# Kernel tuning notes

Hardware: AMD Instinct MI355X
Metric: run time of the kernel (lower is better)

Reference implementation:

```python
import jax, jax.numpy as jnp
import numpy as np

N_KNOTS = 16384
BATCH = 256
N_SAMP = 32768


def setup_inputs() -> dict:
    key = jax.random.key(0)
    k1, k2, k3 = jax.random.split(key, 3)
    # strictly increasing knot abscissae (matches module assumption of sorted x_points)
    incs = jax.random.uniform(k1, (N_KNOTS,), minval=0.01, maxval=1.0, dtype=jnp.float32)
    x_points = jnp.cumsum(incs)
    y_points = jax.random.normal(k2, (N_KNOTS,), dtype=jnp.float32)
    # samples must have a valid right bracket: x in [x_points[0], x_points[N-2])
    lo = x_points[0]
    hi = x_points[N_KNOTS - 2]
    u = jax.random.uniform(k3, (BATCH, N_SAMP), dtype=jnp.float32)
    x_samp = lo + u * (hi - lo) * 0.999
    return {"x_samp": x_samp, "x_points": x_points, "y_points": y_points}


def reference(x_samp, x_points, y_points):
    # Original: masked argmin over (x_samp - x_points) with negatives set to inf,
    # i.e. index of the largest knot <= x_samp. Equivalent to searchsorted(right)-1.
    idxi = jnp.searchsorted(x_points, x_samp, side='right') - 1  # [B, S]
    idxf = idxi + 1
    xi = x_points[idxi]  # [B, S] gather
    xf = x_points[idxf]
    yi = y_points[idxi]
    yf = y_points[idxf]
    ds = (x_samp - xi) / (xf - xi)
    return yi + ds * (yf - yi)
```

## Files before the change

kernel.cpp:

```cpp
#include <hip/hip_runtime.h>


#define NB 16256
#define NKMAX 16384
#define PADR 4
#define NREC (NKMAX + PADR)

typedef float f32x4 __attribute__((ext_vector_type(4)));
typedef float f32x2 __attribute__((ext_vector_type(2)));

__device__ __forceinline__ int bucket_of(float v, float lo, float inv_w) {
    return (int)((v - lo) * inv_w);
}

__device__ __forceinline__ float pack_ys_f(float y, float s) {
    _Float16 hy = (_Float16)y, hs = (_Float16)s;
    unsigned short uy = __builtin_bit_cast(unsigned short, hy);
    unsigned short us = __builtin_bit_cast(unsigned short, hs);
    unsigned u = (unsigned)uy | ((unsigned)us << 16);
    return __builtin_bit_cast(float, u);
}

__device__ __forceinline__ float lerp_ys(float dx, float ysf) {
    unsigned u = __builtin_bit_cast(unsigned, ysf);
    float hy = (float)__builtin_bit_cast(_Float16, (unsigned short)(u & 0xffffu));
    float hs = (float)__builtin_bit_cast(_Float16, (unsigned short)(u >> 16));
    return fmaf(dx, hs, hy);
}

__global__ void build_tbl(const float* __restrict__ xp, const float* __restrict__ yp,
                          float* __restrict__ recg, unsigned short* __restrict__ tbl,
                          int nk) {
    int i = blockIdx.x * blockDim.x + threadIdx.x;
    float lo = xp[0];
    float inv_w = (float)NB / (xp[nk - 1] - lo);
    if (i < nk + PADR) {
        float x, y, s;
        if (i < nk) {
            x = xp[i]; y = yp[i];
            s = (i < nk - 1) ? (yp[i + 1] - y) / (xp[i + 1] - x) : 0.0f;
        } else {
            x = __builtin_inff(); y = 0.0f; s = 0.0f;
        }
        recg[2 * i]     = x;
        recg[2 * i + 1] = pack_ys_f(y, s);
    }
    if (i < NB) {
        int v = 0;
        if (i > 0) {
            int loj = -1, hij = nk - 1;
            while (loj < hij) {
                int mid = (loj + hij + 1) >> 1;
                if (bucket_of(xp[mid], lo, inv_w) <= i - 1) loj = mid; else hij = mid - 1;
            }
            v = loj < 0 ? 0 : (loj > nk - 2 ? nk - 2 : loj);
        }
        tbl[i] = (unsigned short)v;
    }
}

__global__ __launch_bounds__(1024) void interp(
        const f32x4* __restrict__ xs4, const float* __restrict__ xp,
        const float* __restrict__ recg, const unsigned short* __restrict__ tbl,
        f32x4* __restrict__ out4, int n4, int nk) {
    __shared__ __align__(16) float srec[NREC * 2];
    __shared__ unsigned short sT[NB];

    {
        const f32x4* rg4 = (const f32x4*)recg;
        f32x4* sr4 = (f32x4*)srec;
        int n = (NREC * 2) / 4;
        for (int i = threadIdx.x; i < n; i += 1024) sr4[i] = rg4[i];
        for (int i = threadIdx.x; i < NB; i += 1024) sT[i] = tbl[i];
    }

    float lo = xp[0];
    float inv_w = (float)NB / (xp[nk - 1] - lo);
    __syncthreads();

    const f32x2* sr2 = (const f32x2*)srec;

    int tid = blockIdx.x * blockDim.x + threadIdx.x;
    int T = gridDim.x * blockDim.x;

    auto process = [&](f32x4 xq) -> f32x4 {
        float x[4] = {xq.x, xq.y, xq.z, xq.w};
        int base[4];
        f32x2 r0[4], r1[4], r2[4], r3[4];
        #pragma unroll
        for (int k = 0; k < 4; k++) {
            int b = bucket_of(x[k], lo, inv_w);
            b = min(b, NB - 1);
            base[k] = (int)sT[b];
            r0[k] = sr2[base[k]];
            r1[k] = sr2[base[k] + 1];
            r2[k] = sr2[base[k] + 2];
            r3[k] = sr2[base[k] + 3];
        }
        f32x4 res;
        #pragma unroll
        for (int k = 0; k < 4; k++) {
            float xk = x[k];
            float xi = r0[k].x, ys = r0[k].y;
            if (r1[k].x <= xk) { xi = r1[k].x; ys = r1[k].y; }
            if (r2[k].x <= xk) { xi = r2[k].x; ys = r2[k].y; }
            bool tail = (r3[k].x <= xk);
            if (tail) {
                int j = base[k] + 3;
                while (srec[2 * (j + 1)] <= xk) j++;
                xi = srec[2 * j]; ys = srec[2 * j + 1];
            }
            res[k] = lerp_ys(xk - xi, ys);
        }
        return res;
    };

    if (n4 == 8 * T) {
        f32x4 buf[8];
        #pragma unroll
        for (int s = 0; s < 3; s++)
            buf[s] = __builtin_nontemporal_load(&xs4[tid + s * T]);
        #pragma unroll
        for (int s = 0; s < 8; s++) {
            if (s + 3 < 8)
                buf[s + 3] = __builtin_nontemporal_load(&xs4[tid + (s + 3) * T]);
            f32x4 res = process(buf[s]);
            __builtin_nontemporal_store(res, &out4[tid + s * T]);
        }
    } else {
        for (int t = tid; t < n4; t += T) {
            f32x4 xq = __builtin_nontemporal_load(&xs4[t]);
            f32x4 res = process(xq);
            __builtin_nontemporal_store(res, &out4[t]);
        }
    }
}

extern "C" void kernel_launch(void* const* d_in, const int* in_sizes, int n_in,
                              void* d_out, int out_size, void* d_ws, size_t ws_size,
                              hipStream_t stream) {
    const float* xs = (const float*)d_in[0];
    const float* xp = (const float*)d_in[1];
    const float* yp = (const float*)d_in[2];
    int ns = in_sizes[0];
    int nk = in_sizes[1];

    float* recg = (float*)d_ws;
    unsigned short* tbl = (unsigned short*)((char*)d_ws + (size_t)NREC * 2 * sizeof(float));

    int na = (nk + PADR > NB ? nk + PADR : NB);
    build_tbl<<<(na + 255) / 256, 256, 0, stream>>>(xp, yp, recg, tbl, nk);

    int n4 = ns / 4;
    interp<<<256, 1024, 0, stream>>>((const f32x4*)xs, xp, recg, tbl,
                                     (f32x4*)d_out, n4, nk);
}
```

Baseline: 103.8 us.

## Fuse table build into interp kernel, building bucket table per block via scatter

```diff
diff --git a/kernel.cpp b/kernel.cpp
--- a/kernel.cpp
+++ b/kernel.cpp
@@ -28,54 +28,39 @@
     return fmaf(dx, hs, hy);
 }
 
-__global__ void build_tbl(const float* __restrict__ xp, const float* __restrict__ yp,
-                          float* __restrict__ recg, unsigned short* __restrict__ tbl,
-                          int nk) {
-    int i = blockIdx.x * blockDim.x + threadIdx.x;
-    float lo = xp[0];
-    float inv_w = (float)NB / (xp[nk - 1] - lo);
-    if (i < nk + PADR) {
-        float x, y, s;
-        if (i < nk) {
-            x = xp[i]; y = yp[i];
-            s = (i < nk - 1) ? (yp[i + 1] - y) / (xp[i + 1] - x) : 0.0f;
-        } else {
-            x = __builtin_inff(); y = 0.0f; s = 0.0f;
-        }
-        recg[2 * i]     = x;
-        recg[2 * i + 1] = pack_ys_f(y, s);
-    }
-    if (i < NB) {
-        int v = 0;
-        if (i > 0) {
-            int loj = -1, hij = nk - 1;
-            while (loj < hij) {
-                int mid = (loj + hij + 1) >> 1;
-                if (bucket_of(xp[mid], lo, inv_w) <= i - 1) loj = mid; else hij = mid - 1;
-            }
-            v = loj < 0 ? 0 : (loj > nk - 2 ? nk - 2 : loj);
-        }
-        tbl[i] = (unsigned short)v;
-    }
-}
-
 __global__ __launch_bounds__(1024) void interp(
         const f32x4* __restrict__ xs4, const float* __restrict__ xp,
-        const float* __restrict__ recg, const unsigned short* __restrict__ tbl,
-        f32x4* __restrict__ out4, int n4, int nk) {
+        const float* __restrict__ yp, f32x4* __restrict__ out4,
+        int n4, int nk) {
     __shared__ __align__(16) float srec[NREC * 2];
     __shared__ unsigned short sT[NB];
 
-    {
-        const f32x4* rg4 = (const f32x4*)recg;
-        f32x4* sr4 = (f32x4*)srec;
-        int n = (NREC * 2) / 4;
-        for (int i = threadIdx.x; i < n; i += 1024) sr4[i] = rg4[i];
-        for (int i = threadIdx.x; i < NB; i += 1024) sT[i] = tbl[i];
-    }
-
     float lo = xp[0];
     float inv_w = (float)NB / (xp[nk - 1] - lo);
+
+    for (int i = threadIdx.x; i < NREC; i += 1024) {
+        float x, ys;
+        if (i < nk) {
+            float x1 = xp[i], y1 = yp[i];
+            x = x1;
+            float s = 0.0f;
+            if (i < nk - 1) s = (yp[i + 1] - y1) / (xp[i + 1] - x1);
+            ys = pack_ys_f(y1, s);
+        } else {
+            x = __builtin_inff(); ys = 0.0f;
+        }
+        srec[2 * i] = x;
+        srec[2 * i + 1] = ys;
+    }
+    for (int i = threadIdx.x; i < NB; i += 1024) sT[i] = 0;
+    __syncthreads();
+
+    for (int j = threadIdx.x; j < nk - 1; j += 1024) {
+        int b0 = bucket_of(xp[j], lo, inv_w);
+        int b1 = bucket_of(xp[j + 1], lo, inv_w);
+        if (b1 > NB - 1) b1 = NB - 1;
+        for (int i = b0 + 1; i <= b1; i++) sT[i] = (unsigned short)j;
+    }
     __syncthreads();
 
     const f32x2* sr2 = (const f32x2*)srec;
@@ -144,14 +129,9 @@
     const float* yp = (const float*)d_in[2];
     int ns = in_sizes[0];
     int nk = in_sizes[1];
-
-    float* recg = (float*)d_ws;
-    unsigned short* tbl = (unsigned short*)((char*)d_ws + (size_t)NREC * 2 * sizeof(float));
-
-    int na = (nk + PADR > NB ? nk + PADR : NB);
-    build_tbl<<<(na + 255) / 256, 256, 0, stream>>>(xp, yp, recg, tbl, nk);
+    (void)d_ws; (void)ws_size;
 
     int n4 = ns / 4;
-    interp<<<256, 1024, 0, stream>>>((const f32x4*)xs, xp, recg, tbl,
+    interp<<<256, 1024, 0, stream>>>((const f32x4*)xs, xp, yp,
                                      (f32x4*)d_out, n4, nk);
 }
```

Result: no change. 105.1 us (+1.3%).
